# Kernel optimization log

Hardware: AMD Instinct MI355X
Metric: run time of the kernel (lower is better)

Reference implementation:

```python
import jax, jax.numpy as jnp
import numpy as np


def setup_inputs() -> dict:
    key = jax.random.key(0)
    k1, k2, k3, k4 = jax.random.split(key, 4)
    bs, N, J, n_feat, n_out = 32, 512, 4, 64, 128
    X = jax.random.normal(k1, (bs, n_feat, N), dtype=jnp.float32)
    W = jax.random.normal(k2, (bs, N, N, J), dtype=jnp.float32)
    # Conv1d(J*n_feat, n_out, kernel_size=1) weights, init N(0, 0.1)
    fc_w = 0.1 * jax.random.normal(k3, (n_out, J * n_feat), dtype=jnp.float32)
    fc_b = 0.1 * jax.random.normal(k4, (n_out,), dtype=jnp.float32)
    mask = jnp.ones((bs, N), dtype=jnp.float32)  # unused by forward, kept for signature parity
    return {"X": X, "W": W, "fc_w": fc_w, "fc_b": fc_b, "N_batch": 32, "mask": mask}


def reference(X, W, fc_w, fc_b, N_batch, mask):
    bs, n_feat, N = X.shape
    J = W.shape[3]
    # graph_oper: out[b, j*n_feat+f, n] = sum_m W[b,n,m,j] * X[b,f,m]
    gx = jnp.einsum('bnmj,bfm->bjfn', W, X)            # [bs, J, n_feat, N]
    x1 = gx.reshape(bs, J * n_feat, N)                  # [bs, J*n_feat, N]
    # Conv1d with kernel size 1 == pointwise linear over channel dim
    y1 = jnp.einsum('oc,bcn->bon', fc_w, x1) + fc_b[None, :, None]  # [bs, n_out, N]
    y = jnp.sum(y1, axis=2)                             # [bs, n_out]
    return y
```

## Files before the change

kernel.cpp:

```cpp
#include <hip/hip_runtime.h>

#define BS   32
#define NF   64
#define NN   512
#define JJ   4
#define NOUT 128
#define CC   256
#define NC   8
#define ROWS 64
#define MJC  2
#define ROW4 512
#define CH4  256

__global__ __launch_bounds__(256) void sumW_kernel(const float4* __restrict__ W4,
                                                   float4* __restrict__ P4) {
    int blk  = blockIdx.x;
    int mjc  = blk & (MJC - 1);
    int rest = blk >> 1;
    int nc   = rest & (NC - 1);
    int b    = rest >> 3;
    int m    = mjc * CH4 + threadIdx.x;

    const float4* p = W4 + ((size_t)(b * NN + nc * ROWS)) * ROW4 + m;
    float4 acc = make_float4(0.f, 0.f, 0.f, 0.f);
#pragma unroll 8
    for (int r = 0; r < ROWS; ++r) {
        float4 v = p[(size_t)r * ROW4];
        acc.x += v.x; acc.y += v.y; acc.z += v.z; acc.w += v.w;
    }
    P4[((size_t)(b * NC + nc)) * ROW4 + m] = acc;
}

__global__ __launch_bounds__(1024) void finish_kernel(const float4* __restrict__ P4,
                                                      const float4* __restrict__ X4,
                                                      const float4* __restrict__ fcw4,
                                                      const float* __restrict__ fcb,
                                                      float* __restrict__ out) {
    __shared__ __align__(16) float S[JJ][16][36];
    __shared__ __align__(16) float4 Fold[NN];
    __shared__ __align__(16) float Tp[16][CC];
    __shared__ __align__(16) float4 Tsum4[CC / 4];

    int b = blockIdx.x;
    int t = threadIdx.x;

    {
        int m = t & (NN - 1);
        int h = t >> 9;
        const float4* pp = P4 + ((size_t)(b * NC + h * 4)) * ROW4 + m;
        float4 a = make_float4(0.f, 0.f, 0.f, 0.f);
#pragma unroll
        for (int k = 0; k < 4; ++k) {
            float4 v = pp[(size_t)k * ROW4];
            a.x += v.x; a.y += v.y; a.z += v.z; a.w += v.w;
        }
        if (h) Fold[m] = a;
        __syncthreads();
        if (!h) {
            float4 o = Fold[m];
            a.x += o.x; a.y += o.y; a.z += o.z; a.w += o.w;
            int seg = m >> 5, i = m & 31;
            S[0][seg][i] = a.x; S[1][seg][i] = a.y;
            S[2][seg][i] = a.z; S[3][seg][i] = a.w;
        }
        __syncthreads();
    }

    {
        int f = t >> 4, seg = t & 15;
        const float4* xp = X4 + ((size_t)(b * NF + f)) * (NN / 4) + seg * 8;
        const float4* s0 = (const float4*)(&S[0][seg][0]);
        const float4* s1 = (const float4*)(&S[1][seg][0]);
        const float4* s2 = (const float4*)(&S[2][seg][0]);
        const float4* s3 = (const float4*)(&S[3][seg][0]);
        float t0 = 0.f, t1 = 0.f, t2 = 0.f, t3 = 0.f;
#pragma unroll
        for (int i = 0; i < 8; ++i) {
            float4 xv = xp[i];
            float4 b0 = s0[i], b1 = s1[i], b2 = s2[i], b3 = s3[i];
            t0 += xv.x * b0.x + xv.y * b0.y + xv.z * b0.z + xv.w * b0.w;
            t1 += xv.x * b1.x + xv.y * b1.y + xv.z * b1.z + xv.w * b1.w;
            t2 += xv.x * b2.x + xv.y * b2.y + xv.z * b2.z + xv.w * b2.w;
            t3 += xv.x * b3.x + xv.y * b3.y + xv.z * b3.z + xv.w * b3.w;
        }
        Tp[seg][0 * NF + f] = t0;
        Tp[seg][1 * NF + f] = t1;
        Tp[seg][2 * NF + f] = t2;
        Tp[seg][3 * NF + f] = t3;
    }
    __syncthreads();

    if (t < CC) {
        float a = 0.f;
#pragma unroll
        for (int s = 0; s < 16; ++s) a += Tp[s][t];
        ((float*)Tsum4)[t] = a;
    }
    __syncthreads();

    {
        int o = t >> 3, k = t & 7;
        const float4* wp = fcw4 + (size_t)o * (CC / 4) + k * 8;
        float acc = 0.f;
#pragma unroll
        for (int u = 0; u < 8; ++u) {
            float4 wv = wp[u];
            float4 sv = Tsum4[k * 8 + u];
            acc += wv.x * sv.x + wv.y * sv.y + wv.z * sv.z + wv.w * sv.w;
        }
        acc += __shfl_down(acc, 4, 8);
        acc += __shfl_down(acc, 2, 8);
        acc += __shfl_down(acc, 1, 8);
        if (k == 0) out[b * NOUT + o] = acc + (float)NN * fcb[o];
    }
}

extern "C" void kernel_launch(void* const* d_in, const int* in_sizes, int n_in,
                              void* d_out, int out_size, void* d_ws, size_t ws_size,
                              hipStream_t stream) {
    const float4* X4   = (const float4*)d_in[0];
    const float4* W4   = (const float4*)d_in[1];
    const float4* fcw4 = (const float4*)d_in[2];
    const float*  fcb  = (const float*)d_in[3];
    float* out = (float*)d_out;

    float4* P4 = (float4*)d_ws;

    sumW_kernel<<<BS * NC * MJC, 256, 0, stream>>>(W4, P4);
    finish_kernel<<<BS, 1024, 0, stream>>>(P4, X4, fcw4, fcb, out);
}
```

Measured before the change: 211.8 us.

## Fuse X and fc_w contractions into W column-sum kernel, add tiny reduce

Each W-summing block now applies the X contraction and the fc_w projection to its own partial column sums. It writes a 128-wide partial output per block, and a small second kernel adds the 16 partials plus the bias. This replaces the 32-block finish kernel, which had low parallelism, and drops the large P4 round trip through memory. The cost is redundant X and fc_w reads and FLOPs, repeated in all 512 blocks.

```diff
diff --git a/kernel.cpp b/kernel.cpp
--- a/kernel.cpp
+++ b/kernel.cpp
@@ -1,118 +1,85 @@
 #include <hip/hip_runtime.h>
 
-#define BS   32
-#define NF   64
-#define NN   512
-#define JJ   4
-#define NOUT 128
-#define CC   256
-#define NC   8
-#define ROWS 64
-#define MJC  2
-#define ROW4 512
-#define CH4  256
+#define BS    32
+#define NF    64
+#define NN    512
+#define JJ    4
+#define NOUT  128
+#define CC    256
+#define NC    8
+#define ROWS  64
+#define MJC   2
+#define ROW4  512
+#define CH4   256
+#define NPART (NC * MJC)
 
-__global__ __launch_bounds__(256) void sumW_kernel(const float4* __restrict__ W4,
-                                                   float4* __restrict__ P4) {
+__global__ __launch_bounds__(256) void fused_kernel(const float4* __restrict__ W4,
+                                                    const float4* __restrict__ X4,
+                                                    const float4* __restrict__ fcw4,
+                                                    float* __restrict__ Yp) {
+    __shared__ __align__(16) float Sl[JJ][260];
+    __shared__ __align__(16) float Tl[CC];
+
     int blk  = blockIdx.x;
     int mjc  = blk & (MJC - 1);
     int rest = blk >> 1;
     int nc   = rest & (NC - 1);
     int b    = rest >> 3;
-    int m    = mjc * CH4 + threadIdx.x;
-
-    const float4* p = W4 + ((size_t)(b * NN + nc * ROWS)) * ROW4 + m;
-    float4 acc = make_float4(0.f, 0.f, 0.f, 0.f);
-#pragma unroll 8
-    for (int r = 0; r < ROWS; ++r) {
-        float4 v = p[(size_t)r * ROW4];
-        acc.x += v.x; acc.y += v.y; acc.z += v.z; acc.w += v.w;
-    }
-    P4[((size_t)(b * NC + nc)) * ROW4 + m] = acc;
-}
-
-__global__ __launch_bounds__(1024) void finish_kernel(const float4* __restrict__ P4,
-                                                      const float4* __restrict__ X4,
-                                                      const float4* __restrict__ fcw4,
-                                                      const float* __restrict__ fcb,
-                                                      float* __restrict__ out) {
-    __shared__ __align__(16) float S[JJ][16][36];
-    __shared__ __align__(16) float4 Fold[NN];
-    __shared__ __align__(16) float Tp[16][CC];
-    __shared__ __align__(16) float4 Tsum4[CC / 4];
-
-    int b = blockIdx.x;
-    int t = threadIdx.x;
+    int t    = threadIdx.x;
+    int m    = mjc * CH4 + t;
 
     {
-        int m = t & (NN - 1);
-        int h = t >> 9;
-        const float4* pp = P4 + ((size_t)(b * NC + h * 4)) * ROW4 + m;
-        float4 a = make_float4(0.f, 0.f, 0.f, 0.f);
-#pragma unroll
-        for (int k = 0; k < 4; ++k) {
-            float4 v = pp[(size_t)k * ROW4];
-            a.x += v.x; a.y += v.y; a.z += v.z; a.w += v.w;
+        const float4* p = W4 + ((size_t)(b * NN + nc * ROWS)) * ROW4 + m;
+        float4 acc = make_float4(0.f, 0.f, 0.f, 0.f);
+#pragma unroll 8
+        for (int r = 0; r < ROWS; ++r) {
+            float4 v = p[(size_t)r * ROW4];
+            acc.x += v.x; acc.y += v.y; acc.z += v.z; acc.w += v.w;
         }
-        if (h) Fold[m] = a;
-        __syncthreads();
-        if (!h) {
-            float4 o = Fold[m];
-            a.x += o.x; a.y += o.y; a.z += o.z; a.w += o.w;
-            int seg = m >> 5, i = m & 31;
-            S[0][seg][i] = a.x; S[1][seg][i] = a.y;
-            S[2][seg][i] = a.z; S[3][seg][i] = a.w;
-        }
-        __syncthreads();
-    }
-
-    {
-        int f = t >> 4, seg = t & 15;
-        const float4* xp = X4 + ((size_t)(b * NF + f)) * (NN / 4) + seg * 8;
-        const float4* s0 = (const float4*)(&S[0][seg][0]);
-        const float4* s1 = (const float4*)(&S[1][seg][0]);
-        const float4* s2 = (const float4*)(&S[2][seg][0]);
-        const float4* s3 = (const float4*)(&S[3][seg][0]);
-        float t0 = 0.f, t1 = 0.f, t2 = 0.f, t3 = 0.f;
-#pragma unroll
-        for (int i = 0; i < 8; ++i) {
-            float4 xv = xp[i];
-            float4 b0 = s0[i], b1 = s1[i], b2 = s2[i], b3 = s3[i];
-            t0 += xv.x * b0.x + xv.y * b0.y + xv.z * b0.z + xv.w * b0.w;
-            t1 += xv.x * b1.x + xv.y * b1.y + xv.z * b1.z + xv.w * b1.w;
-            t2 += xv.x * b2.x + xv.y * b2.y + xv.z * b2.z + xv.w * b2.w;
-            t3 += xv.x * b3.x + xv.y * b3.y + xv.z * b3.z + xv.w * b3.w;
-        }
-        Tp[seg][0 * NF + f] = t0;
-        Tp[seg][1 * NF + f] = t1;
-        Tp[seg][2 * NF + f] = t2;
-        Tp[seg][3 * NF + f] = t3;
-    }
-    __syncthreads();
-
-    if (t < CC) {
-        float a = 0.f;
-#pragma unroll
-        for (int s = 0; s < 16; ++s) a += Tp[s][t];
-        ((float*)Tsum4)[t] = a;
+        Sl[0][t] = acc.x; Sl[1][t] = acc.y; Sl[2][t] = acc.z; Sl[3][t] = acc.w;
     }
     __syncthreads();
 
     {
-        int o = t >> 3, k = t & 7;
-        const float4* wp = fcw4 + (size_t)o * (CC / 4) + k * 8;
-        float acc = 0.f;
+        int j = t & 3, f = t >> 2;
+        const float4* xp = X4 + ((size_t)(b * NF + f)) * (NN / 4) + mjc * (CH4 / 4);
+        const float4* sp = (const float4*)(&Sl[j][0]);
+        float tp = 0.f;
 #pragma unroll
-        for (int u = 0; u < 8; ++u) {
+        for (int i = 0; i < CH4 / 4; ++i) {
+            float4 xv = xp[i];
+            float4 sv = sp[i];
+            tp += xv.x * sv.x + xv.y * sv.y + xv.z * sv.z + xv.w * sv.w;
+        }
+        Tl[j * NF + f] = tp;
+    }
+    __syncthreads();
+
+    {
+        int o = t >> 1, h = t & 1;
+        const float4* wp  = fcw4 + (size_t)o * (CC / 4) + h * 32;
+        const float4* tl4 = (const float4*)Tl;
+        float a = 0.f;
+#pragma unroll
+        for (int u = 0; u < 32; ++u) {
             float4 wv = wp[u];
-            float4 sv = Tsum4[k * 8 + u];
-            acc += wv.x * sv.x + wv.y * sv.y + wv.z * sv.z + wv.w * sv.w;
+            float4 tv = tl4[h * 32 + u];
+            a += wv.x * tv.x + wv.y * tv.y + wv.z * tv.z + wv.w * tv.w;
         }
-        acc += __shfl_down(acc, 4, 8);
-        acc += __shfl_down(acc, 2, 8);
-        acc += __shfl_down(acc, 1, 8);
-        if (k == 0) out[b * NOUT + o] = acc + (float)NN * fcb[o];
+        a += __shfl_down(a, 1, 2);
+        if (!h) Yp[(size_t)blk * NOUT + o] = a;
     }
+}
+
+__global__ __launch_bounds__(128) void reduce_kernel(const float* __restrict__ Yp,
+                                                     const float* __restrict__ fcb,
+                                                     float* __restrict__ out) {
+    int b = blockIdx.x, o = threadIdx.x;
+    float a = (float)NN * fcb[o];
+    const float* pp = Yp + (size_t)b * NPART * NOUT + o;
+#pragma unroll
+    for (int q = 0; q < NPART; ++q) a += pp[q * NOUT];
+    out[b * NOUT + o] = a;
 }
 
 extern "C" void kernel_launch(void* const* d_in, const int* in_sizes, int n_in,
@@ -124,8 +91,8 @@
     const float*  fcb  = (const float*)d_in[3];
     float* out = (float*)d_out;
 
-    float4* P4 = (float4*)d_ws;
+    float* Yp = (float*)d_ws;
 
-    sumW_kernel<<<BS * NC * MJC, 256, 0, stream>>>(W4, P4);
-    finish_kernel<<<BS, 1024, 0, stream>>>(P4, X4, fcw4, fcb, out);
+    fused_kernel<<<BS * NC * MJC, 256, 0, stream>>>(W4, X4, fcw4, Yp);
+    reduce_kernel<<<BS, 128, 0, stream>>>(Yp, fcb, out);
 }
```

Measured after the change: 213.4 us. Within noise of the previous version (+0.7%).
